# Kernel tuning notes

Hardware: AMD Instinct MI355X
Metric: run time of the kernel (lower is better)

## Reference

```python
import jax, jax.numpy as jnp
import numpy as np

N_NODES = 100000


def high_pass_filter(z, src, dst, n):
    # add self loops (PyG add_self_loops appends [i, i] edges)
    loop = jnp.arange(n, dtype=src.dtype)
    src2 = jnp.concatenate([src, loop])
    dst2 = jnp.concatenate([dst, loop])
    ones = jnp.ones(src2.shape[0], dtype=z.dtype)
    # deg = degree(edge_index[0]) -> out-degree counts per source node
    deg = jax.ops.segment_sum(ones, src2, num_segments=n)
    # mean aggregation at target nodes: out[i] = mean_{(j->i)} z[j]
    msg_sum = jax.ops.segment_sum(z[src2], dst2, num_segments=n)
    cnt = jax.ops.segment_sum(ones, dst2, num_segments=n)
    mean_out = msg_sum / cnt[:, None]  # cnt >= 1 thanks to self loops
    return z - mean_out / deg[:, None]


def setup_inputs() -> dict:
    key = jax.random.key(0)
    k = jax.random.split(key, 8)
    d = 64
    E = 1200000
    x = jax.random.normal(k[0], (N_NODES, d), dtype=jnp.float32)
    edge_index = jax.random.randint(k[1], (2, E), 0, N_NODES, dtype=jnp.int64)
    s = 1.0 / np.sqrt(d)
    W1 = jax.random.uniform(k[2], (d, d), jnp.float32, -s, s)
    b1 = jax.random.uniform(k[3], (d,), jnp.float32, -s, s)
    W2 = jax.random.uniform(k[4], (d, d), jnp.float32, -s, s)
    b2 = jax.random.uniform(k[5], (d,), jnp.float32, -s, s)
    W3 = jax.random.uniform(k[6], (d, d), jnp.float32, -s, s)
    b3 = jax.random.uniform(k[7], (d,), jnp.float32, -s, s)
    return {"x": x, "edge_index": edge_index, "W1": W1, "b1": b1,
            "W2": W2, "b2": b2, "W3": W3, "b3": b3}


def reference(x, edge_index, W1, b1, W2, b2, W3, b3):
    src, dst = edge_index[0], edge_index[1]
    n = x.shape[0]
    z = jax.nn.relu(x @ W1 + b1)
    z = high_pass_filter(z, src, dst, n)
    z = jax.nn.relu(z @ W2 + b2)
    z = high_pass_filter(z, src, dst, n)
    z = jax.nn.relu(z @ W3 + b3)
    return z
```

## Files before the change

### kernel.cpp

```cpp
#include <hip/hip_runtime.h>

#define D 64
#define CAP 48
#define CAPB 3584
#define BIN_CHUNK 2048
#define LDS_STRIDE 68

typedef unsigned int uint;
typedef unsigned short ushort;

__device__ __forceinline__ ushort f2bf(float f) {
    uint u = __float_as_uint(f);
    return (ushort)((u + 0x7FFFu + ((u >> 16) & 1u)) >> 16);
}

#define SWZ(c, k4) ((((k4) ^ (((c) >> 2) & 7)) << 2))

__global__ void k_zero(int* __restrict__ p, int n) {
    int i = blockIdx.x * blockDim.x + threadIdx.x;
    if (i < n) p[i] = 0;
}

__global__ __launch_bounds__(256) void k_bin2(
    const int* __restrict__ src, const int* __restrict__ dst, int E, int nb,
    int* __restrict__ gcur, int* __restrict__ binD, int* __restrict__ binS)
{
    __shared__ int curD[512], curS[512];
    const int t = threadIdx.x;
    for (int i = t; i < nb; i += 256) { curD[i] = 0; curS[i] = 0; }
    __syncthreads();

    const int e0 = blockIdx.x * BIN_CHUNK;
    int sv[8], dv[8];
#pragma unroll
    for (int i = 0; i < 8; ++i) {
        int e = e0 + i * 256 + t;
        if (e < E) {
            sv[i] = src[e]; dv[i] = dst[e];
            atomicAdd(&curD[dv[i] >> 8], 1);
            atomicAdd(&curS[sv[i] >> 8], 1);
        } else {
            sv[i] = -1;
        }
    }
    __syncthreads();
    for (int i = t; i < nb; i += 256) {
        int c = curD[i]; curD[i] = c ? atomicAdd(&gcur[i], c) : 0;
        c = curS[i];     curS[i] = c ? atomicAdd(&gcur[nb + i], c) : 0;
    }
    __syncthreads();
#pragma unroll
    for (int i = 0; i < 8; ++i) {
        if (sv[i] >= 0) {
            int b = dv[i] >> 8;
            int pos = atomicAdd(&curD[b], 1);
            if (pos < CAPB) binD[(size_t)b * CAPB + pos] = ((dv[i] & 255) << 17) | sv[i];
            b = sv[i] >> 8;
            pos = atomicAdd(&curS[b], 1);
            if (pos < CAPB) binS[(size_t)b * CAPB + pos] = sv[i] & 255;
        }
    }
}

__device__ void gemm_body(const float* z, const float* __restrict__ W,
                          const float* __restrict__ bias, float* out,
                          ushort* zh_out, int n, float* sX, float* sWT, int tile)
{
    const int t = threadIdx.x;
    const int row0 = tile << 6;

    for (int i = 0; i < 4; ++i) {
        int s = i * 256 + t;
        int k = s >> 4;
        int c4 = (s & 15) << 2;
        float4 w = ((const float4*)W)[s];
        int kk = SWZ(c4 + 0, k >> 2) + (k & 3);
        sWT[(c4 + 0) * LDS_STRIDE + kk] = w.x;
        kk = SWZ(c4 + 1, k >> 2) + (k & 3);
        sWT[(c4 + 1) * LDS_STRIDE + kk] = w.y;
        kk = SWZ(c4 + 2, k >> 2) + (k & 3);
        sWT[(c4 + 2) * LDS_STRIDE + kk] = w.z;
        kk = SWZ(c4 + 3, k >> 2) + (k & 3);
        sWT[(c4 + 3) * LDS_STRIDE + kk] = w.w;
    }
    for (int i = 0; i < 4; ++i) {
        int s = i * 256 + t;
        int r = s >> 4;
        int grow = row0 + r;
        float4 v = make_float4(0.f, 0.f, 0.f, 0.f);
        if (grow < n) v = ((const float4*)(z + (size_t)grow * D))[s & 15];
        *((float4*)(sX + r * LDS_STRIDE + ((s & 15) << 2))) = v;
    }
    __syncthreads();

    const int tc = (t & 15) << 2;
    const int tr = (t >> 4) << 2;

    float acc[4][4] = {};
#define DOT4(a_, w_, acc_) \
    acc_ = fmaf((a_).x, (w_).x, fmaf((a_).y, (w_).y, fmaf((a_).z, (w_).z, fmaf((a_).w, (w_).w, acc_))))
    for (int k4 = 0; k4 < 16; ++k4) {
        float4 a0 = *(const float4*)(sX + (tr + 0) * LDS_STRIDE + (k4 << 2));
        float4 a1 = *(const float4*)(sX + (tr + 1) * LDS_STRIDE + (k4 << 2));
        float4 a2 = *(const float4*)(sX + (tr + 2) * LDS_STRIDE + (k4 << 2));
        float4 a3 = *(const float4*)(sX + (tr + 3) * LDS_STRIDE + (k4 << 2));
        float4 w0 = *(const float4*)(sWT + (tc + 0) * LDS_STRIDE + SWZ(tc + 0, k4));
        float4 w1 = *(const float4*)(sWT + (tc + 1) * LDS_STRIDE + SWZ(tc + 1, k4));
        float4 w2 = *(const float4*)(sWT + (tc + 2) * LDS_STRIDE + SWZ(tc + 2, k4));
        float4 w3 = *(const float4*)(sWT + (tc + 3) * LDS_STRIDE + SWZ(tc + 3, k4));
        DOT4(a0, w0, acc[0][0]); DOT4(a0, w1, acc[0][1]); DOT4(a0, w2, acc[0][2]); DOT4(a0, w3, acc[0][3]);
        DOT4(a1, w0, acc[1][0]); DOT4(a1, w1, acc[1][1]); DOT4(a1, w2, acc[1][2]); DOT4(a1, w3, acc[1][3]);
        DOT4(a2, w0, acc[2][0]); DOT4(a2, w1, acc[2][1]); DOT4(a2, w2, acc[2][2]); DOT4(a2, w3, acc[2][3]);
        DOT4(a3, w0, acc[3][0]); DOT4(a3, w1, acc[3][1]); DOT4(a3, w2, acc[3][2]); DOT4(a3, w3, acc[3][3]);
    }
#undef DOT4

    float b0 = bias[tc + 0], b1 = bias[tc + 1], b2 = bias[tc + 2], b3 = bias[tc + 3];
    for (int rr = 0; rr < 4; ++rr) {
        int grow = row0 + tr + rr;
        if (grow >= n) continue;
        float4 o;
        o.x = fmaxf(acc[rr][0] + b0, 0.f);
        o.y = fmaxf(acc[rr][1] + b1, 0.f);
        o.z = fmaxf(acc[rr][2] + b2, 0.f);
        o.w = fmaxf(acc[rr][3] + b3, 0.f);
        ((float4*)(out + (size_t)grow * D))[tc >> 2] = o;
        if (zh_out) {
            short4 h;
            h.x = (short)f2bf(o.x); h.y = (short)f2bf(o.y);
            h.z = (short)f2bf(o.z); h.w = (short)f2bf(o.w);
            *(short4*)(zh_out + (size_t)grow * D + tc) = h;
        }
    }
}

__global__ __launch_bounds__(256) void k_finishG(
    const int* __restrict__ gcur, const int* __restrict__ binD,
    const int* __restrict__ binS, int n, int nb,
    int* __restrict__ csr, int* __restrict__ icnt, float* __restrict__ inv,
    const float* __restrict__ x, const float* __restrict__ W1,
    const float* __restrict__ b1, float* __restrict__ zA,
    ushort* __restrict__ zh, int ntiles)
{
    __shared__ float smem[2 * 64 * LDS_STRIDE];
    if (blockIdx.x >= nb) {
        gemm_body(x, W1, b1, zA, zh, n, smem, smem + 64 * LDS_STRIDE,
                  blockIdx.x - nb);
        return;
    }
    int* cur = (int*)smem;
    int* od  = (int*)smem + 256;
    const int b = blockIdx.x, t = threadIdx.x;
    cur[t] = 0; od[t] = 0;
    __syncthreads();

    int cntD = gcur[b]; if (cntD > CAPB) cntD = CAPB;
    const int* bb = binD + (size_t)b * CAPB;
    for (int i = t; i < cntD; i += 256) {
        int v = bb[i];
        int dloc = v >> 17;
        int pos = atomicAdd(&cur[dloc], 1);
        if (pos < CAP) csr[(size_t)((b << 8) + dloc) * CAP + pos] = v & 0x1FFFF;
    }
    int cntS = gcur[nb + b]; if (cntS > CAPB) cntS = CAPB;
    const int* bs = binS + (size_t)b * CAPB;
    for (int i = t; i < cntS; i += 256) {
        atomicAdd(&od[bs[i]], 1);
    }
    __syncthreads();
    int node = (b << 8) + t;
    if (node < n) {
        int ic = cur[t]; if (ic > CAP) ic = CAP;
        icnt[node] = ic;
        inv[node] = 1.0f / ((float)(od[t] + 1) * (float)(ic + 1));
    }
}

__global__ __launch_bounds__(256) void k_gemm(
    const float* z, const float* __restrict__ W, const float* __restrict__ bias,
    float* out, ushort* zh_out, int n)
{
    __shared__ float smem[2 * 64 * LDS_STRIDE];
    gemm_body(z, W, bias, out, zh_out, n, smem, smem + 64 * LDS_STRIDE, blockIdx.x);
}

__global__ __launch_bounds__(256) void k_aggr(
    const float* __restrict__ zA, const ushort* __restrict__ zh,
    const int* __restrict__ icnt, const int* __restrict__ csr,
    const float* __restrict__ inv, int n, float* __restrict__ zB)
{
    int w = (blockIdx.x * 256 + threadIdx.x) >> 6;
    int lane = threadIdx.x & 63;
    int c8 = (lane & 7) << 3;
    int j = lane >> 3;
    if (w >= n) return;

    int cnt = icnt[w]; if (cnt > CAP) cnt = CAP;
    int my = (lane < cnt) ? csr[w * CAP + lane] : 0;
    int nit = (cnt + 7) >> 3;

    float iv = 0.f;
    float4 s0 = make_float4(0.f, 0.f, 0.f, 0.f);
    float4 s1 = make_float4(0.f, 0.f, 0.f, 0.f);
    if (j == 0) {
        iv = inv[w];
        const float* zr = zA + (size_t)w * D + c8;
        s0 = *(const float4*)zr;
        s1 = *(const float4*)(zr + 4);
    }

    float a[8] = {0.f, 0.f, 0.f, 0.f, 0.f, 0.f, 0.f, 0.f};
    for (int it = 0; it < nit; ++it) {
        int e = (it << 3) + j;
        int s = __shfl(my, e, 64);
        uint4 u = *(const uint4*)(zh + (size_t)s * D + c8);
        if (e < cnt) {
            a[0] += __uint_as_float(u.x << 16);
            a[1] += __uint_as_float(u.x & 0xFFFF0000u);
            a[2] += __uint_as_float(u.y << 16);
            a[3] += __uint_as_float(u.y & 0xFFFF0000u);
            a[4] += __uint_as_float(u.z << 16);
            a[5] += __uint_as_float(u.z & 0xFFFF0000u);
            a[6] += __uint_as_float(u.w << 16);
            a[7] += __uint_as_float(u.w & 0xFFFF0000u);
        }
    }
#pragma unroll
    for (int m = 8; m <= 32; m <<= 1) {
#pragma unroll
        for (int i = 0; i < 8; ++i) a[i] += __shfl_xor(a[i], m, 64);
    }

    if (j == 0) {
        float4 o0, o1;
        o0.x = fmaf(-(a[0] + s0.x), iv, s0.x);
        o0.y = fmaf(-(a[1] + s0.y), iv, s0.y);
        o0.z = fmaf(-(a[2] + s0.z), iv, s0.z);
        o0.w = fmaf(-(a[3] + s0.w), iv, s0.w);
        o1.x = fmaf(-(a[4] + s1.x), iv, s1.x);
        o1.y = fmaf(-(a[5] + s1.y), iv, s1.y);
        o1.z = fmaf(-(a[6] + s1.z), iv, s1.z);
        o1.w = fmaf(-(a[7] + s1.w), iv, s1.w);
        float* zo = zB + (size_t)w * D + c8;
        *(float4*)zo = o0;
        *(float4*)(zo + 4) = o1;
    }
}

extern "C" void kernel_launch(void* const* d_in, const int* in_sizes, int n_in,
                              void* d_out, int out_size, void* d_ws, size_t ws_size,
                              hipStream_t stream) {
    const float* x  = (const float*)d_in[0];
    const int*   ei = (const int*)d_in[1];
    const float* W1 = (const float*)d_in[2];
    const float* b1 = (const float*)d_in[3];
    const float* W2 = (const float*)d_in[4];
    const float* b2 = (const float*)d_in[5];
    const float* W3 = (const float*)d_in[6];
    const float* b3 = (const float*)d_in[7];

    const int n = in_sizes[0] / D;
    const int E = in_sizes[1] / 2;
    const int* src = ei;
    const int* dst = ei + E;

    const int nb = (n + 255) >> 8;

    float*  zA   = (float*)d_ws;
    ushort* zh   = (ushort*)(zA + (size_t)n * D);
    float*  inv  = (float*)(zh + (size_t)n * D);
    int*    icnt = (int*)(inv + n);
    int*    csr  = icnt + n;
    int*    gcur = csr + (size_t)n * CAP;
    int*    binD = gcur + 2 * nb;
    int*    binS = binD + (size_t)nb * CAPB;

    float* out = (float*)d_out;
    dim3 blk(256);

    const int bin_blocks = (E + BIN_CHUNK - 1) / BIN_CHUNK;
    const int ntiles = (n + 63) >> 6;

    k_zero<<<dim3((2 * nb + 255) / 256), blk, 0, stream>>>(gcur, 2 * nb);
    k_bin2<<<dim3(bin_blocks), blk, 0, stream>>>(src, dst, E, nb, gcur, binD, binS);
    k_finishG<<<dim3(nb + ntiles), blk, 0, stream>>>(
        gcur, binD, binS, n, nb, csr, icnt, inv, x, W1, b1, zA, zh, ntiles);

    dim3 gemm_grid(ntiles);
    dim3 aggr_grid((n + 3) / 4);

    k_aggr<<<aggr_grid, blk, 0, stream>>>(zA, zh, icnt, csr, inv, n, zA);
    k_gemm<<<gemm_grid, blk, 0, stream>>>(zA, W2, b2, zA, zh, n);
    k_aggr<<<aggr_grid, blk, 0, stream>>>(zA, zh, icnt, csr, inv, n, zA);
    k_gemm<<<gemm_grid, blk, 0, stream>>>(zA, W3, b3, out, nullptr, n);
}
```

Measured before the change: 264.0 us.

## Stage binned edges in LDS for coalesced writes; aggregate four nodes per wave

The binning kernel now computes a block-local prefix scan of bin counts and stages edge records in shared memory sorted by bin. Each bin's entries are then written contiguously to global memory, replacing scattered per-edge writes. The aggregation kernel processes four destination nodes per wavefront and issues four independent gathers per iteration to raise memory-level parallelism. The costs are extra synchronisation and scans in binning, and more registers plus padding iterations up to the maximum degree among the four nodes in aggregation.

```diff
diff --git a/kernel.cpp b/kernel.cpp
--- a/kernel.cpp
+++ b/kernel.cpp
@@ -25,9 +25,10 @@
     const int* __restrict__ src, const int* __restrict__ dst, int E, int nb,
     int* __restrict__ gcur, int* __restrict__ binD, int* __restrict__ binS)
 {
-    __shared__ int curD[512], curS[512];
+    __shared__ int hD[512], hS[512], sc[512], cur2[512];
+    __shared__ int sdata[BIN_CHUNK], sdest[BIN_CHUNK];
     const int t = threadIdx.x;
-    for (int i = t; i < nb; i += 256) { curD[i] = 0; curS[i] = 0; }
+    hD[t] = 0; hD[t + 256] = 0; hS[t] = 0; hS[t + 256] = 0;
     __syncthreads();
 
     const int e0 = blockIdx.x * BIN_CHUNK;
@@ -37,28 +38,81 @@
         int e = e0 + i * 256 + t;
         if (e < E) {
             sv[i] = src[e]; dv[i] = dst[e];
-            atomicAdd(&curD[dv[i] >> 8], 1);
-            atomicAdd(&curS[sv[i] >> 8], 1);
+            atomicAdd(&hD[dv[i] >> 8], 1);
+            atomicAdd(&hS[sv[i] >> 8], 1);
         } else {
             sv[i] = -1;
         }
     }
     __syncthreads();
-    for (int i = t; i < nb; i += 256) {
-        int c = curD[i]; curD[i] = c ? atomicAdd(&gcur[i], c) : 0;
-        c = curS[i];     curS[i] = c ? atomicAdd(&gcur[nb + i], c) : 0;
+
+    int nvalid = E - e0; if (nvalid > BIN_CHUNK) nvalid = BIN_CHUNK;
+
+    sc[t] = hD[t]; sc[t + 256] = hD[t + 256];
+    __syncthreads();
+    for (int off = 1; off < 512; off <<= 1) {
+        int v0 = (t >= off) ? sc[t - off] : 0;
+        int v1 = ((t + 256) >= off) ? sc[t + 256 - off] : 0;
+        __syncthreads();
+        sc[t] += v0; sc[t + 256] += v1;
+        __syncthreads();
+    }
+    for (int k = t; k < 512; k += 256) {
+        int h = hD[k];
+        int lb = sc[k] - h;
+        cur2[k] = lb;
+        int go = (k < nb && h) ? atomicAdd(&gcur[k], h) : 0;
+        sc[k] = k * CAPB + go - lb;
     }
     __syncthreads();
 #pragma unroll
     for (int i = 0; i < 8; ++i) {
         if (sv[i] >= 0) {
             int b = dv[i] >> 8;
-            int pos = atomicAdd(&curD[b], 1);
-            if (pos < CAPB) binD[(size_t)b * CAPB + pos] = ((dv[i] & 255) << 17) | sv[i];
-            b = sv[i] >> 8;
-            pos = atomicAdd(&curS[b], 1);
-            if (pos < CAPB) binS[(size_t)b * CAPB + pos] = sv[i] & 255;
-        }
+            int pos = atomicAdd(&cur2[b], 1);
+            int dabs = sc[b] + pos;
+            sdata[pos] = ((dv[i] & 255) << 17) | sv[i];
+            sdest[pos] = (dabs - b * CAPB < CAPB) ? dabs : -1;
+        }
+    }
+    __syncthreads();
+    for (int i = t; i < nvalid; i += 256) {
+        int d2 = sdest[i];
+        if (d2 >= 0) binD[d2] = sdata[i];
+    }
+    __syncthreads();
+
+    sc[t] = hS[t]; sc[t + 256] = hS[t + 256];
+    __syncthreads();
+    for (int off = 1; off < 512; off <<= 1) {
+        int v0 = (t >= off) ? sc[t - off] : 0;
+        int v1 = ((t + 256) >= off) ? sc[t + 256 - off] : 0;
+        __syncthreads();
+        sc[t] += v0; sc[t + 256] += v1;
+        __syncthreads();
+    }
+    for (int k = t; k < 512; k += 256) {
+        int h = hS[k];
+        int lb = sc[k] - h;
+        cur2[k] = lb;
+        int go = (k < nb && h) ? atomicAdd(&gcur[nb + k], h) : 0;
+        sc[k] = k * CAPB + go - lb;
+    }
+    __syncthreads();
+#pragma unroll
+    for (int i = 0; i < 8; ++i) {
+        if (sv[i] >= 0) {
+            int b = sv[i] >> 8;
+            int pos = atomicAdd(&cur2[b], 1);
+            int dabs = sc[b] + pos;
+            sdata[pos] = sv[i] & 255;
+            sdest[pos] = (dabs - b * CAPB < CAPB) ? dabs : -1;
+        }
+    }
+    __syncthreads();
+    for (int i = t; i < nvalid; i += 256) {
+        int d2 = sdest[i];
+        if (d2 >= 0) binS[d2] = sdata[i];
     }
 }
 
@@ -184,66 +238,86 @@
     gemm_body(z, W, bias, out, zh_out, n, smem, smem + 64 * LDS_STRIDE, blockIdx.x);
 }
 
+#define ACC8(a_, u_) do { \
+    (a_)[0] += __uint_as_float((u_).x << 16); \
+    (a_)[1] += __uint_as_float((u_).x & 0xFFFF0000u); \
+    (a_)[2] += __uint_as_float((u_).y << 16); \
+    (a_)[3] += __uint_as_float((u_).y & 0xFFFF0000u); \
+    (a_)[4] += __uint_as_float((u_).z << 16); \
+    (a_)[5] += __uint_as_float((u_).z & 0xFFFF0000u); \
+    (a_)[6] += __uint_as_float((u_).w << 16); \
+    (a_)[7] += __uint_as_float((u_).w & 0xFFFF0000u); \
+} while (0)
+
 __global__ __launch_bounds__(256) void k_aggr(
     const float* __restrict__ zA, const ushort* __restrict__ zh,
     const int* __restrict__ icnt, const int* __restrict__ csr,
     const float* __restrict__ inv, int n, float* __restrict__ zB)
 {
-    int w = (blockIdx.x * 256 + threadIdx.x) >> 6;
+    int q = (blockIdx.x * 256 + threadIdx.x) >> 6;
     int lane = threadIdx.x & 63;
     int c8 = (lane & 7) << 3;
     int j = lane >> 3;
-    if (w >= n) return;
-
-    int cnt = icnt[w]; if (cnt > CAP) cnt = CAP;
-    int my = (lane < cnt) ? csr[w * CAP + lane] : 0;
-    int nit = (cnt + 7) >> 3;
-
-    float iv = 0.f;
-    float4 s0 = make_float4(0.f, 0.f, 0.f, 0.f);
-    float4 s1 = make_float4(0.f, 0.f, 0.f, 0.f);
-    if (j == 0) {
-        iv = inv[w];
-        const float* zr = zA + (size_t)w * D + c8;
-        s0 = *(const float4*)zr;
-        s1 = *(const float4*)(zr + 4);
-    }
-
-    float a[8] = {0.f, 0.f, 0.f, 0.f, 0.f, 0.f, 0.f, 0.f};
+    int w0 = q << 2;
+    if (w0 >= n) return;
+
+    int cnt[4], my[4];
+    int maxc = 0;
+#pragma unroll
+    for (int p = 0; p < 4; ++p) {
+        int w = w0 + p;
+        int c = (w < n) ? icnt[w] : 0; if (c > CAP) c = CAP;
+        cnt[p] = c; if (c > maxc) maxc = c;
+        my[p] = (lane < c) ? csr[w * CAP + lane] : 0;
+    }
+    int nit = (maxc + 7) >> 3;
+
+    float a[4][8] = {};
     for (int it = 0; it < nit; ++it) {
         int e = (it << 3) + j;
-        int s = __shfl(my, e, 64);
-        uint4 u = *(const uint4*)(zh + (size_t)s * D + c8);
-        if (e < cnt) {
-            a[0] += __uint_as_float(u.x << 16);
-            a[1] += __uint_as_float(u.x & 0xFFFF0000u);
-            a[2] += __uint_as_float(u.y << 16);
-            a[3] += __uint_as_float(u.y & 0xFFFF0000u);
-            a[4] += __uint_as_float(u.z << 16);
-            a[5] += __uint_as_float(u.z & 0xFFFF0000u);
-            a[6] += __uint_as_float(u.w << 16);
-            a[7] += __uint_as_float(u.w & 0xFFFF0000u);
-        }
+        int s0 = __shfl(my[0], e, 64);
+        int s1 = __shfl(my[1], e, 64);
+        int s2 = __shfl(my[2], e, 64);
+        int s3 = __shfl(my[3], e, 64);
+        uint4 u0 = *(const uint4*)(zh + (size_t)s0 * D + c8);
+        uint4 u1 = *(const uint4*)(zh + (size_t)s1 * D + c8);
+        uint4 u2 = *(const uint4*)(zh + (size_t)s2 * D + c8);
+        uint4 u3 = *(const uint4*)(zh + (size_t)s3 * D + c8);
+        if (e < cnt[0]) ACC8(a[0], u0);
+        if (e < cnt[1]) ACC8(a[1], u1);
+        if (e < cnt[2]) ACC8(a[2], u2);
+        if (e < cnt[3]) ACC8(a[3], u3);
     }
 #pragma unroll
     for (int m = 8; m <= 32; m <<= 1) {
 #pragma unroll
-        for (int i = 0; i < 8; ++i) a[i] += __shfl_xor(a[i], m, 64);
+        for (int p = 0; p < 4; ++p)
+#pragma unroll
+            for (int i = 0; i < 8; ++i) a[p][i] += __shfl_xor(a[p][i], m, 64);
     }
 
     if (j == 0) {
-        float4 o0, o1;
-        o0.x = fmaf(-(a[0] + s0.x), iv, s0.x);
-        o0.y = fmaf(-(a[1] + s0.y), iv, s0.y);
-        o0.z = fmaf(-(a[2] + s0.z), iv, s0.z);
-        o0.w = fmaf(-(a[3] + s0.w), iv, s0.w);
-        o1.x = fmaf(-(a[4] + s1.x), iv, s1.x);
-        o1.y = fmaf(-(a[5] + s1.y), iv, s1.y);
-        o1.z = fmaf(-(a[6] + s1.z), iv, s1.z);
-        o1.w = fmaf(-(a[7] + s1.w), iv, s1.w);
-        float* zo = zB + (size_t)w * D + c8;
-        *(float4*)zo = o0;
-        *(float4*)(zo + 4) = o1;
+#pragma unroll
+        for (int p = 0; p < 4; ++p) {
+            int w = w0 + p;
+            if (w >= n) break;
+            float iv = inv[w];
+            const float* zr = zA + (size_t)w * D + c8;
+            float4 s0 = *(const float4*)zr;
+            float4 s1 = *(const float4*)(zr + 4);
+            float4 o0, o1;
+            o0.x = fmaf(-(a[p][0] + s0.x), iv, s0.x);
+            o0.y = fmaf(-(a[p][1] + s0.y), iv, s0.y);
+            o0.z = fmaf(-(a[p][2] + s0.z), iv, s0.z);
+            o0.w = fmaf(-(a[p][3] + s0.w), iv, s0.w);
+            o1.x = fmaf(-(a[p][4] + s1.x), iv, s1.x);
+            o1.y = fmaf(-(a[p][5] + s1.y), iv, s1.y);
+            o1.z = fmaf(-(a[p][6] + s1.z), iv, s1.z);
+            o1.w = fmaf(-(a[p][7] + s1.w), iv, s1.w);
+            float* zo = zB + (size_t)w * D + c8;
+            *(float4*)zo = o0;
+            *(float4*)(zo + 4) = o1;
+        }
     }
 }
 
@@ -287,7 +361,7 @@
         gcur, binD, binS, n, nb, csr, icnt, inv, x, W1, b1, zA, zh, ntiles);
 
     dim3 gemm_grid(ntiles);
-    dim3 aggr_grid((n + 3) / 4);
+    dim3 aggr_grid((n + 15) / 16);
 
     k_aggr<<<aggr_grid, blk, 0, stream>>>(zA, zh, icnt, csr, inv, n, zA);
     k_gemm<<<gemm_grid, blk, 0, stream>>>(zA, W2, b2, zA, zh, n);
```

New measurement: 280.7 us. +6.3%, slower.
